# Optimization experiments

Hardware: AMD Instinct MI355X
Metric: run time of the kernel (lower is better)

## Reference

```python
import jax, jax.numpy as jnp
import numpy as np
import math

B, Q, K = 2, 2048, 2048
C_Q = C_K = C_V = 256
H, D = 8, 32  # no_heads, c_hidden


def setup_inputs() -> dict:
    key = jax.random.key(0)
    ks = jax.random.split(key, 9)
    s_in = 1.0 / math.sqrt(C_Q)
    return {
        "q_x": jax.random.normal(ks[0], (B, Q, C_Q), jnp.float32),
        "kv_x": jax.random.normal(ks[1], (B, K, C_K), jnp.float32),
        "bias": jax.random.normal(ks[2], (B, 1, Q, K), jnp.float32),
        # projection weights, stored torch-style as [out, in]
        "Wq": jax.random.normal(ks[3], (H * D, C_Q), jnp.float32) * s_in,
        "Wk": jax.random.normal(ks[4], (H * D, C_K), jnp.float32) * s_in,
        "Wv": jax.random.normal(ks[5], (H * D, C_V), jnp.float32) * s_in,
        "Wo": jax.random.normal(ks[6], (C_Q, H * D), jnp.float32) * (1.0 / math.sqrt(H * D)),
        "bo": jnp.zeros((C_Q,), jnp.float32),
        "Wg": jax.random.normal(ks[7], (H * D, C_Q), jnp.float32) * 0.02,
        "bg": jnp.ones((H * D,), jnp.float32),
    }


def reference(q_x, kv_x, bias, Wq, Wk, Wv, Wo, bo, Wg, bg):
    inv_sqrt_d = 1.0 / math.sqrt(D)
    # project and split heads: [B, S, H, D]
    q = (q_x @ Wq.T).reshape(B, Q, H, D) * inv_sqrt_d
    k = (kv_x @ Wk.T).reshape(B, K, H, D)
    v = (kv_x @ Wv.T).reshape(B, K, H, D)
    # scores [B, H, Q, K] with broadcast bias
    a = jnp.einsum("bqhd,bkhd->bhqk", q, k) + bias
    a = jax.nn.softmax(a, axis=-1)
    # attend: [B, Q, H, D]
    o = jnp.einsum("bhqk,bkhd->bqhd", a, v)
    # output gating from query data
    g = jax.nn.sigmoid(q_x @ Wg.T + bg).reshape(B, Q, H, D)
    o = o * g
    o = o.reshape(B, Q, H * D)
    return o @ Wo.T + bo
```

## Files before the change

### kernel.cpp

```cpp
#include <hip/hip_runtime.h>
#include <hip/hip_bf16.h>

#define SEQ 2048
#define H_ 8
#define D_ 32

typedef __attribute__((ext_vector_type(4))) short short4v;
typedef __attribute__((ext_vector_type(8))) short short8v;
typedef __attribute__((ext_vector_type(4))) float floatx4;

static __device__ __forceinline__ unsigned short f2bf(float f) {
  union { float f; unsigned u; } v; v.f = f;
  unsigned r = v.u + 0x7fff + ((v.u >> 16) & 1);
  return (unsigned short)(r >> 16);
}
static __device__ __forceinline__ float bf2f(unsigned short h) {
  union { unsigned u; float f; } v; v.u = ((unsigned)h) << 16; return v.f;
}
static __device__ __forceinline__ int pd(int d) {
  return ((d & 12) << 1) | (d & 3) | ((d & 16) >> 2);
}

__global__ __launch_bounds__(256) void prep_w(const float* wq, const float* wk,
                                              const float* wv, const float* wg,
                                              const float* wo, unsigned short* o) {
  int i = blockIdx.x * 256 + threadIdx.x;
  int m = i >> 16, j = i & 65535;
  int n = j >> 8, k = j & 255;
  const float* s = (m == 0) ? wq : (m == 1) ? wk : (m == 2) ? wv : (m == 3) ? wg : wo;
  o[(m << 16) + n * 256 + ((k & ~31) | pd(k & 31))] = f2bf(s[j]);
}

#define XS_STRIDE 264
__global__ __launch_bounds__(512) void proj_kernel(
    const float* qx, const float* kvx, const unsigned short* wbf,
    const unsigned short* ao,
    unsigned short* qp, unsigned short* kp, unsigned short* vt,
    unsigned short* gate, const float* bg, float* outp, const float* bo,
    int ms_base) {
  __shared__ unsigned short xs[16 * XS_STRIDE];
  const int ms = ms_base + blockIdx.y;
  const int tid = threadIdx.x;
  const int lane = tid & 63;
  const int wid = tid >> 6;
  const int m0 = blockIdx.x * 16;
  const int g = lane >> 4, l15 = lane & 15;

  {
    int row = tid >> 5, rem = tid & 31, kb = rem >> 2, qd = rem & 3;
    int koff = kb * 32 + qd * 4;
    unsigned short* dst = xs + row * XS_STRIDE + kb * 32 + qd * 8;
    if (ms < 2) {
      const float* X = ((ms == 0) ? qx : kvx) + (m0 + row) * 256 + koff;
      floatx4 f0 = *(const floatx4*)X;
      floatx4 f1 = *(const floatx4*)(X + 16);
      short8v sv;
#pragma unroll
      for (int j = 0; j < 4; ++j) {
        sv[j] = (short)f2bf(f0[j]);
        sv[4 + j] = (short)f2bf(f1[j]);
      }
      *(short8v*)dst = sv;
    } else {
      const unsigned short* A = ao + (m0 + row) * 256 + koff;
      short4v a0 = *(const short4v*)A;
      short4v a1 = *(const short4v*)(A + 16);
      *(short8v*)dst = __builtin_shufflevector(a0, a1, 0, 1, 2, 3, 4, 5, 6, 7);
    }
  }
  __syncthreads();

  const int NT = (ms < 2) ? 4 : 2;
  const unsigned short* wsel;
  int nbase;
  if (ms == 0) {
    wsel = (wid < 4) ? wbf : wbf + 3 * 65536;
    nbase = (wid & 3) * 64;
  } else if (ms == 1) {
    wsel = (wid < 4) ? wbf + 1 * 65536 : wbf + 2 * 65536;
    nbase = (wid & 3) * 64;
  } else {
    wsel = wbf + 4 * 65536;
    nbase = wid * 32;
  }

  floatx4 acc[4];
#pragma unroll
  for (int nt = 0; nt < 4; ++nt) {
    floatx4 z = {0.f, 0.f, 0.f, 0.f};
    acc[nt] = z;
  }

#pragma unroll
  for (int ks = 0; ks < 8; ++ks) {
    short8v A = *(short8v*)(xs + l15 * XS_STRIDE + ks * 32 + 8 * g);
#pragma unroll
    for (int nt = 0; nt < 4; ++nt) {
      if (nt < NT) {
        int n = nbase + nt * 16 + l15;
        short8v Bf = *(const short8v*)(wsel + n * 256 + ks * 32 + 8 * g);
        acc[nt] = __builtin_amdgcn_mfma_f32_16x16x32_bf16(A, Bf, acc[nt], 0, 0, 0);
      }
    }
  }

  const int b = m0 >> 11;
  const int s0r = m0 & 2047;
#pragma unroll
  for (int nt = 0; nt < 4; ++nt) {
    if (nt >= NT) break;
    int n = nbase + nt * 16 + l15;
    if (ms == 0) {
      if (wid < 4) {
        int h = n >> 5, d = n & 31;
        unsigned short* dst = qp + ((b * H_ + h) * SEQ + s0r + 4 * g) * D_ + pd(d);
#pragma unroll
        for (int r = 0; r < 4; ++r)
          dst[r * D_] = f2bf(acc[nt][r] * 0.17677669529663687f);
      } else {
#pragma unroll
        for (int r = 0; r < 4; ++r) {
          float sg = 1.f / (1.f + __expf(-(acc[nt][r] + bg[n])));
          gate[(b * SEQ + s0r + 4 * g + r) * 256 + n] = f2bf(sg);
        }
      }
    } else if (ms == 1) {
      if (wid < 4) {
        int h = n >> 5, d = n & 31;
        unsigned short* dst = kp + ((b * H_ + h) * SEQ + s0r + 4 * g) * D_ + pd(d);
#pragma unroll
        for (int r = 0; r < 4; ++r)
          dst[r * D_] = f2bf(acc[nt][r]);
      } else {
        int h = n >> 5, d = n & 31;
        int sb = (s0r & ~31) + 8 * g + ((m0 & 16) ? 4 : 0);
        short4v vv;
#pragma unroll
        for (int r = 0; r < 4; ++r) vv[r] = (short)f2bf(acc[nt][r]);
        *(short4v*)(vt + ((b * H_ + h) * D_ + d) * SEQ + sb) = vv;
      }
    } else {
#pragma unroll
      for (int r = 0; r < 4; ++r)
        outp[(m0 + 4 * g + r) * 256 + n] = acc[nt][r] + bo[n];
    }
  }
}

__global__ __launch_bounds__(512) void attn_kernel(
    const unsigned short* qp, const unsigned short* kp, const unsigned short* vt,
    const unsigned short* gate, const float* bias, unsigned short* ao) {
  const int tid = threadIdx.x;
  const int lane = tid & 63;
  const int h = tid >> 6;
  const int b = blockIdx.y;
  const int q0 = blockIdx.x * 16;
  const int g = lane >> 4, l15 = lane & 15;

  short8v qfrag = *(const short8v*)(qp + ((b * H_ + h) * SEQ + q0 + l15) * D_ + 8 * g);
  const unsigned short* kpb = kp + (b * H_ + h) * SEQ * D_;
  const unsigned short* vtb = vt + (b * H_ + h) * D_ * SEQ;
  const float* biasb = bias + (b * SEQ + q0 + l15) * SEQ;

  floatx4 o0 = {0.f, 0.f, 0.f, 0.f}, o1 = {0.f, 0.f, 0.f, 0.f};
  float lacc = 0.f;

#pragma unroll 2
  for (int k0 = 0; k0 < SEQ; k0 += 32) {
    short8v kf0 = *(const short8v*)(kpb + (k0 + l15) * D_ + 8 * g);
    short8v kf1 = *(const short8v*)(kpb + (k0 + 16 + l15) * D_ + 8 * g);
    floatx4 z = {0.f, 0.f, 0.f, 0.f};
    floatx4 s0 = __builtin_amdgcn_mfma_f32_16x16x32_bf16(kf0, qfrag, z, 0, 0, 0);
    floatx4 s1 = __builtin_amdgcn_mfma_f32_16x16x32_bf16(kf1, qfrag, z, 0, 0, 0);
    floatx4 bv0 = *(const floatx4*)(biasb + k0 + 4 * g);
    floatx4 bv1 = *(const floatx4*)(biasb + k0 + 16 + 4 * g);
    short8v pf;
#pragma unroll
    for (int r = 0; r < 4; ++r) {
      float p0 = __expf(s0[r] + bv0[r]);
      float p1 = __expf(s1[r] + bv1[r]);
      lacc += p0 + p1;
      pf[r] = (short)f2bf(p0);
      pf[4 + r] = (short)f2bf(p1);
    }
    short8v vf0 = *(const short8v*)(vtb + l15 * SEQ + k0 + 8 * g);
    short8v vf1 = *(const short8v*)(vtb + (16 + l15) * SEQ + k0 + 8 * g);
    o0 = __builtin_amdgcn_mfma_f32_16x16x32_bf16(vf0, pf, o0, 0, 0, 0);
    o1 = __builtin_amdgcn_mfma_f32_16x16x32_bf16(vf1, pf, o1, 0, 0, 0);
  }

  lacc += __shfl_xor(lacc, 16, 64);
  lacc += __shfl_xor(lacc, 32, 64);
  float inv_l = 1.f / lacc;

  int q = q0 + l15;
  const unsigned short* gb = gate + (b * SEQ + q) * 256 + h * D_;
  unsigned short* aob = ao + (b * SEQ + q) * 256 + h * D_;
#pragma unroll
  for (int dt = 0; dt < 2; ++dt) {
    floatx4 oo = dt ? o1 : o0;
    short4v gv = *(const short4v*)(gb + dt * 16 + 4 * g);
    short4v ov;
#pragma unroll
    for (int r = 0; r < 4; ++r) {
      float o = oo[r] * inv_l * bf2f((unsigned short)gv[r]);
      ov[r] = (short)f2bf(o);
    }
    *(short4v*)(aob + dt * 16 + 4 * g) = ov;
  }
}

extern "C" void kernel_launch(void* const* d_in, const int* in_sizes, int n_in,
                              void* d_out, int out_size, void* d_ws, size_t ws_size,
                              hipStream_t stream) {
  const float* qx = (const float*)d_in[0];
  const float* kvx = (const float*)d_in[1];
  const float* bias = (const float*)d_in[2];
  const float* Wq = (const float*)d_in[3];
  const float* Wk = (const float*)d_in[4];
  const float* Wv = (const float*)d_in[5];
  const float* Wo = (const float*)d_in[6];
  const float* bo = (const float*)d_in[7];
  const float* Wg = (const float*)d_in[8];
  const float* bg = (const float*)d_in[9];
  float* out = (float*)d_out;

  unsigned short* ws = (unsigned short*)d_ws;
  unsigned short* wbf = ws;
  unsigned short* qp = ws + 327680;
  unsigned short* kp = qp + 1048576;
  unsigned short* vt = kp + 1048576;
  unsigned short* gate = vt + 1048576;
  unsigned short* ao = gate + 1048576;

  prep_w<<<dim3(1280), dim3(256), 0, stream>>>(Wq, Wk, Wv, Wg, Wo, wbf);
  proj_kernel<<<dim3(256, 2), dim3(512), 0, stream>>>(qx, kvx, wbf, ao, qp, kp, vt,
                                                      gate, bg, out, bo, 0);
  attn_kernel<<<dim3(128, 2), dim3(512), 0, stream>>>(qp, kp, vt, gate, bias, ao);
  proj_kernel<<<dim3(256, 1), dim3(512), 0, stream>>>(qx, kvx, wbf, ao, qp, kp, vt,
                                                      gate, bg, out, bo, 2);
}
```

Before: 189.2 us.

## Split attention over key chunks with reduction kernel and restructure projection GEMMs

Attention is split across four key chunks (grid z), giving four times as many blocks to fill the GPU. Each chunk writes partial outputs and partial softmax sums to fp32 workspace, and a new reduce kernel combines them and applies the gate. The inputs are converted to bf16 in a separate prep pass. The projection GEMMs are rewritten so each wave keeps its weight fragments in registers and loops over four M tiles. This adds extra kernel launches and partial-result traffic to global memory in exchange for better occupancy. Softmax still uses exp without a max subtraction, so splitting keeps the math consistent.

```diff
diff --git a/kernel.cpp b/kernel.cpp
--- a/kernel.cpp
+++ b/kernel.cpp
@@ -4,6 +4,8 @@
 #define SEQ 2048
 #define H_ 8
 #define D_ 32
+#define SPLIT 4
+#define KCHUNK 512
 
 typedef __attribute__((ext_vector_type(4))) short short4v;
 typedef __attribute__((ext_vector_type(8))) short short8v;
@@ -21,140 +23,102 @@
   return ((d & 12) << 1) | (d & 3) | ((d & 16) >> 2);
 }
 
-__global__ __launch_bounds__(256) void prep_w(const float* wq, const float* wk,
-                                              const float* wv, const float* wg,
-                                              const float* wo, unsigned short* o) {
-  int i = blockIdx.x * 256 + threadIdx.x;
-  int m = i >> 16, j = i & 65535;
-  int n = j >> 8, k = j & 255;
-  const float* s = (m == 0) ? wq : (m == 1) ? wk : (m == 2) ? wv : (m == 3) ? wg : wo;
-  o[(m << 16) + n * 256 + ((k & ~31) | pd(k & 31))] = f2bf(s[j]);
-}
-
-#define XS_STRIDE 264
-__global__ __launch_bounds__(512) void proj_kernel(
-    const float* qx, const float* kvx, const unsigned short* wbf,
-    const unsigned short* ao,
-    unsigned short* qp, unsigned short* kp, unsigned short* vt,
-    unsigned short* gate, const float* bg, float* outp, const float* bo,
-    int ms_base) {
-  __shared__ unsigned short xs[16 * XS_STRIDE];
-  const int ms = ms_base + blockIdx.y;
-  const int tid = threadIdx.x;
-  const int lane = tid & 63;
-  const int wid = tid >> 6;
-  const int m0 = blockIdx.x * 16;
+__global__ __launch_bounds__(256) void prep_all(
+    const float* wq, const float* wk, const float* wv, const float* wg,
+    const float* wo, const float* qx, const float* kvx,
+    unsigned short* wbf, unsigned short* xqb, unsigned short* xkb) {
+  if (blockIdx.x < 1280) {
+    int i = blockIdx.x * 256 + threadIdx.x;
+    int m = i >> 16, j = i & 65535;
+    int n = j >> 8, k = j & 255;
+    const float* s = (m == 0) ? wq : (m == 1) ? wk : (m == 2) ? wv : (m == 3) ? wg : wo;
+    wbf[(m << 16) + n * 256 + ((k & ~31) | pd(k & 31))] = f2bf(s[j]);
+  } else {
+    int i = (blockIdx.x - 1280) * 256 + threadIdx.x;
+    int m = i >> 18;
+    int j = (i & 262143) * 4;
+    const float* X = m ? kvx : qx;
+    unsigned short* O = m ? xkb : xqb;
+    floatx4 f = *(const floatx4*)(X + j);
+    int row = j >> 8, k = j & 255;
+    int base = row * 256 + (k & ~31) + ((k & 12) << 1) + ((k & 16) >> 2);
+    short4v s;
+#pragma unroll
+    for (int r = 0; r < 4; ++r) s[r] = (short)f2bf(f[r]);
+    *(short4v*)(O + base) = s;
+  }
+}
+
+__global__ __launch_bounds__(256) void proj_qkvg(
+    const unsigned short* xqb, const unsigned short* xkb,
+    const unsigned short* wbf, unsigned short* qp, unsigned short* kp,
+    unsigned short* vt, unsigned short* gate, const float* bg) {
+  const int gw = blockIdx.x * 4 + (threadIdx.x >> 6);
+  const int lane = threadIdx.x & 63;
   const int g = lane >> 4, l15 = lane & 15;
-
-  {
-    int row = tid >> 5, rem = tid & 31, kb = rem >> 2, qd = rem & 3;
-    int koff = kb * 32 + qd * 4;
-    unsigned short* dst = xs + row * XS_STRIDE + kb * 32 + qd * 8;
-    if (ms < 2) {
-      const float* X = ((ms == 0) ? qx : kvx) + (m0 + row) * 256 + koff;
-      floatx4 f0 = *(const floatx4*)X;
-      floatx4 f1 = *(const floatx4*)(X + 16);
-      short8v sv;
-#pragma unroll
-      for (int j = 0; j < 4; ++j) {
-        sv[j] = (short)f2bf(f0[j]);
-        sv[4 + j] = (short)f2bf(f1[j]);
+  const int sel = gw >> 10;
+  const int nchunk = (gw >> 6) & 15;
+  const int mgroup = gw & 63;
+  const unsigned short* xb = (sel < 2) ? xqb : xkb;
+  const unsigned short* wsel =
+      wbf + ((sel == 0) ? 0 : (sel == 1) ? 3 : (sel == 2) ? 1 : 2) * 65536;
+  const int n = nchunk * 16 + l15;
+
+  short8v w[8];
+#pragma unroll
+  for (int ks = 0; ks < 8; ++ks)
+    w[ks] = *(const short8v*)(wsel + n * 256 + ks * 32 + 8 * g);
+
+#pragma unroll
+  for (int mt = 0; mt < 4; ++mt) {
+    int row0 = mgroup * 64 + mt * 16;
+    floatx4 acc = {0.f, 0.f, 0.f, 0.f};
+#pragma unroll
+    for (int ks = 0; ks < 8; ++ks) {
+      short8v A = *(const short8v*)(xb + (row0 + l15) * 256 + ks * 32 + 8 * g);
+      acc = __builtin_amdgcn_mfma_f32_16x16x32_bf16(A, w[ks], acc, 0, 0, 0);
+    }
+    int b = row0 >> 11, s = row0 & 2047;
+    if (sel == 0) {
+      int h = n >> 5, d = n & 31;
+      unsigned short* dst = qp + ((b * H_ + h) * SEQ + s + 4 * g) * D_ + pd(d);
+#pragma unroll
+      for (int r = 0; r < 4; ++r)
+        dst[r * D_] = f2bf(acc[r] * 0.17677669529663687f);
+    } else if (sel == 1) {
+      float bgn = bg[n];
+#pragma unroll
+      for (int r = 0; r < 4; ++r) {
+        float sg = 1.f / (1.f + __expf(-(acc[r] + bgn)));
+        gate[(b * SEQ + s + 4 * g + r) * 256 + n] = f2bf(sg);
       }
-      *(short8v*)dst = sv;
+    } else if (sel == 2) {
+      int h = n >> 5, d = n & 31;
+      unsigned short* dst = kp + ((b * H_ + h) * SEQ + s + 4 * g) * D_ + pd(d);
+#pragma unroll
+      for (int r = 0; r < 4; ++r)
+        dst[r * D_] = f2bf(acc[r]);
     } else {
-      const unsigned short* A = ao + (m0 + row) * 256 + koff;
-      short4v a0 = *(const short4v*)A;
-      short4v a1 = *(const short4v*)(A + 16);
-      *(short8v*)dst = __builtin_shufflevector(a0, a1, 0, 1, 2, 3, 4, 5, 6, 7);
-    }
-  }
-  __syncthreads();
-
-  const int NT = (ms < 2) ? 4 : 2;
-  const unsigned short* wsel;
-  int nbase;
-  if (ms == 0) {
-    wsel = (wid < 4) ? wbf : wbf + 3 * 65536;
-    nbase = (wid & 3) * 64;
-  } else if (ms == 1) {
-    wsel = (wid < 4) ? wbf + 1 * 65536 : wbf + 2 * 65536;
-    nbase = (wid & 3) * 64;
-  } else {
-    wsel = wbf + 4 * 65536;
-    nbase = wid * 32;
-  }
-
-  floatx4 acc[4];
-#pragma unroll
-  for (int nt = 0; nt < 4; ++nt) {
-    floatx4 z = {0.f, 0.f, 0.f, 0.f};
-    acc[nt] = z;
-  }
-
-#pragma unroll
-  for (int ks = 0; ks < 8; ++ks) {
-    short8v A = *(short8v*)(xs + l15 * XS_STRIDE + ks * 32 + 8 * g);
-#pragma unroll
-    for (int nt = 0; nt < 4; ++nt) {
-      if (nt < NT) {
-        int n = nbase + nt * 16 + l15;
-        short8v Bf = *(const short8v*)(wsel + n * 256 + ks * 32 + 8 * g);
-        acc[nt] = __builtin_amdgcn_mfma_f32_16x16x32_bf16(A, Bf, acc[nt], 0, 0, 0);
-      }
-    }
-  }
-
-  const int b = m0 >> 11;
-  const int s0r = m0 & 2047;
-#pragma unroll
-  for (int nt = 0; nt < 4; ++nt) {
-    if (nt >= NT) break;
-    int n = nbase + nt * 16 + l15;
-    if (ms == 0) {
-      if (wid < 4) {
-        int h = n >> 5, d = n & 31;
-        unsigned short* dst = qp + ((b * H_ + h) * SEQ + s0r + 4 * g) * D_ + pd(d);
-#pragma unroll
-        for (int r = 0; r < 4; ++r)
-          dst[r * D_] = f2bf(acc[nt][r] * 0.17677669529663687f);
-      } else {
-#pragma unroll
-        for (int r = 0; r < 4; ++r) {
-          float sg = 1.f / (1.f + __expf(-(acc[nt][r] + bg[n])));
-          gate[(b * SEQ + s0r + 4 * g + r) * 256 + n] = f2bf(sg);
-        }
-      }
-    } else if (ms == 1) {
-      if (wid < 4) {
-        int h = n >> 5, d = n & 31;
-        unsigned short* dst = kp + ((b * H_ + h) * SEQ + s0r + 4 * g) * D_ + pd(d);
-#pragma unroll
-        for (int r = 0; r < 4; ++r)
-          dst[r * D_] = f2bf(acc[nt][r]);
-      } else {
-        int h = n >> 5, d = n & 31;
-        int sb = (s0r & ~31) + 8 * g + ((m0 & 16) ? 4 : 0);
-        short4v vv;
-#pragma unroll
-        for (int r = 0; r < 4; ++r) vv[r] = (short)f2bf(acc[nt][r]);
-        *(short4v*)(vt + ((b * H_ + h) * D_ + d) * SEQ + sb) = vv;
-      }
-    } else {
-#pragma unroll
-      for (int r = 0; r < 4; ++r)
-        outp[(m0 + 4 * g + r) * 256 + n] = acc[nt][r] + bo[n];
+      int h = n >> 5, d = n & 31;
+      int sb = (s & ~31) + 8 * g + ((row0 & 16) ? 4 : 0);
+      short4v vv;
+#pragma unroll
+      for (int r = 0; r < 4; ++r) vv[r] = (short)f2bf(acc[r]);
+      *(short4v*)(vt + ((b * H_ + h) * D_ + d) * SEQ + sb) = vv;
     }
   }
 }
 
 __global__ __launch_bounds__(512) void attn_kernel(
     const unsigned short* qp, const unsigned short* kp, const unsigned short* vt,
-    const unsigned short* gate, const float* bias, unsigned short* ao) {
+    const float* bias, float* po, float* pl) {
   const int tid = threadIdx.x;
   const int lane = tid & 63;
   const int h = tid >> 6;
   const int b = blockIdx.y;
-  const int q0 = blockIdx.x * 16;
+  const int qt = blockIdx.x;
+  const int chunk = blockIdx.z;
+  const int q0 = qt * 16;
   const int g = lane >> 4, l15 = lane & 15;
 
   short8v qfrag = *(const short8v*)(qp + ((b * H_ + h) * SEQ + q0 + l15) * D_ + 8 * g);
@@ -165,8 +129,9 @@
   floatx4 o0 = {0.f, 0.f, 0.f, 0.f}, o1 = {0.f, 0.f, 0.f, 0.f};
   float lacc = 0.f;
 
+  const int kbeg = chunk * KCHUNK;
 #pragma unroll 2
-  for (int k0 = 0; k0 < SEQ; k0 += 32) {
+  for (int k0 = kbeg; k0 < kbeg + KCHUNK; k0 += 32) {
     short8v kf0 = *(const short8v*)(kpb + (k0 + l15) * D_ + 8 * g);
     short8v kf1 = *(const short8v*)(kpb + (k0 + 16 + l15) * D_ + 8 * g);
     floatx4 z = {0.f, 0.f, 0.f, 0.f};
@@ -191,22 +156,68 @@
 
   lacc += __shfl_xor(lacc, 16, 64);
   lacc += __shfl_xor(lacc, 32, 64);
-  float inv_l = 1.f / lacc;
-
-  int q = q0 + l15;
-  const unsigned short* gb = gate + (b * SEQ + q) * 256 + h * D_;
-  unsigned short* aob = ao + (b * SEQ + q) * 256 + h * D_;
-#pragma unroll
-  for (int dt = 0; dt < 2; ++dt) {
-    floatx4 oo = dt ? o1 : o0;
-    short4v gv = *(const short4v*)(gb + dt * 16 + 4 * g);
-    short4v ov;
-#pragma unroll
-    for (int r = 0; r < 4; ++r) {
-      float o = oo[r] * inv_l * bf2f((unsigned short)gv[r]);
-      ov[r] = (short)f2bf(o);
-    }
-    *(short4v*)(aob + dt * 16 + 4 * g) = ov;
+
+  const int widg = ((chunk * 2 + b) * H_ + h) * 128 + qt;
+  float* pob = po + (size_t)widg * 512;
+  *(floatx4*)(pob + lane * 8) = o0;
+  *(floatx4*)(pob + lane * 8 + 4) = o1;
+  if (lane < 16) pl[widg * 16 + l15] = lacc;
+}
+
+__global__ __launch_bounds__(512) void reduce_kernel(
+    const float* po, const float* pl, const unsigned short* gate,
+    unsigned short* ao) {
+  const int bh = blockIdx.x;
+  const int qt = bh & 127;
+  const int h = (bh >> 7) & 7;
+  const int b = bh >> 10;
+  const int j = threadIdx.x;
+  const int lane_s = j >> 3, e = j & 7;
+  const int q = lane_s & 15;
+
+  float o = 0.f, l = 0.f;
+#pragma unroll
+  for (int c = 0; c < SPLIT; ++c) {
+    int widg = ((c * 2 + b) * H_ + h) * 128 + qt;
+    o += po[(size_t)widg * 512 + j];
+    l += pl[widg * 16 + q];
+  }
+  int dt = e >> 2, r = e & 3, g = lane_s >> 4;
+  int d = dt * 16 + 4 * g + r;
+  int s = qt * 16 + q;
+  float gv = bf2f(gate[(b * SEQ + s) * 256 + h * D_ + d]);
+  ao[(b * SEQ + s) * 256 + h * D_ + pd(d)] = f2bf(o / l * gv);
+}
+
+__global__ __launch_bounds__(256) void proj_out(
+    const unsigned short* ao, const unsigned short* wbf, float* outp,
+    const float* bo) {
+  const int gw = blockIdx.x * 4 + (threadIdx.x >> 6);
+  const int lane = threadIdx.x & 63;
+  const int g = lane >> 4, l15 = lane & 15;
+  const int nchunk = gw >> 6;
+  const int mgroup = gw & 63;
+  const unsigned short* wsel = wbf + 4 * 65536;
+  const int n = nchunk * 16 + l15;
+
+  short8v w[8];
+#pragma unroll
+  for (int ks = 0; ks < 8; ++ks)
+    w[ks] = *(const short8v*)(wsel + n * 256 + ks * 32 + 8 * g);
+  float bon = bo[n];
+
+#pragma unroll
+  for (int mt = 0; mt < 4; ++mt) {
+    int row0 = mgroup * 64 + mt * 16;
+    floatx4 acc = {0.f, 0.f, 0.f, 0.f};
+#pragma unroll
+    for (int ks = 0; ks < 8; ++ks) {
+      short8v A = *(const short8v*)(ao + (row0 + l15) * 256 + ks * 32 + 8 * g);
+      acc = __builtin_amdgcn_mfma_f32_16x16x32_bf16(A, w[ks], acc, 0, 0, 0);
+    }
+#pragma unroll
+    for (int r = 0; r < 4; ++r)
+      outp[(row0 + 4 * g + r) * 256 + n] = acc[r] + bon;
   }
 }
 
@@ -227,16 +238,22 @@
 
   unsigned short* ws = (unsigned short*)d_ws;
   unsigned short* wbf = ws;
-  unsigned short* qp = ws + 327680;
+  unsigned short* xqb = ws + 327680;
+  unsigned short* xkb = xqb + 1048576;
+  unsigned short* qp = xkb + 1048576;
   unsigned short* kp = qp + 1048576;
   unsigned short* vt = kp + 1048576;
   unsigned short* gate = vt + 1048576;
   unsigned short* ao = gate + 1048576;
-
-  prep_w<<<dim3(1280), dim3(256), 0, stream>>>(Wq, Wk, Wv, Wg, Wo, wbf);
-  proj_kernel<<<dim3(256, 2), dim3(512), 0, stream>>>(qx, kvx, wbf, ao, qp, kp, vt,
-                                                      gate, bg, out, bo, 0);
-  attn_kernel<<<dim3(128, 2), dim3(512), 0, stream>>>(qp, kp, vt, gate, bias, ao);
-  proj_kernel<<<dim3(256, 1), dim3(512), 0, stream>>>(qx, kvx, wbf, ao, qp, kp, vt,
-                                                      gate, bg, out, bo, 2);
-}
+  float* po = (float*)(ao + 1048576);
+  float* pl = po + (size_t)SPLIT * 2 * H_ * 128 * 512;
+
+  prep_all<<<dim3(3328), dim3(256), 0, stream>>>(Wq, Wk, Wv, Wg, Wo, qx, kvx,
+                                                 wbf, xqb, xkb);
+  proj_qkvg<<<dim3(1024), dim3(256), 0, stream>>>(xqb, xkb, wbf, qp, kp, vt,
+                                                  gate, bg);
+  attn_kernel<<<dim3(128, 2, SPLIT), dim3(512), 0, stream>>>(qp, kp, vt, bias,
+                                                             po, pl);
+  reduce_kernel<<<dim3(2048), dim3(512), 0, stream>>>(po, pl, gate, ao);
+  proj_out<<<dim3(256), dim3(256), 0, stream>>>(ao, wbf, out, bo);
+}
```

Measured after the change: 199.6 us. +5.5%, slower.
